# Kernel tuning notes

Hardware: AMD Instinct MI355X
Metric: run time of the kernel (lower is better)

Reference implementation:

```python
import jax, jax.numpy as jnp
import numpy as np

N_NODES = 50000


def gat_layer(x, src, dst, W, att_s, att_d, b, concat):
    # PyG GATConv (eval mode): h = x W reshaped to [N, H, C]
    H, C = att_s.shape
    h = (x @ W).reshape(-1, H, C)                      # [N, H, C]
    a_s = (h * att_s).sum(-1)                          # [N, H]
    a_d = (h * att_d).sum(-1)                          # [N, H]
    e = jax.nn.leaky_relu(a_s[src] + a_d[dst], 0.2)    # [E, H]
    # scatter-softmax over destination nodes
    m = jax.ops.segment_max(e, dst, num_segments=N_NODES)
    alpha = jnp.exp(e - m[dst])
    denom = jax.ops.segment_sum(alpha, dst, num_segments=N_NODES)
    alpha = alpha / denom[dst]                         # [E, H]
    msg = h[src] * alpha[:, :, None]                   # [E, H, C]
    out = jax.ops.segment_sum(msg, dst, num_segments=N_NODES)  # [N, H, C]
    out = out.reshape(N_NODES, H * C) if concat else out.mean(axis=1)
    return out + b


def setup_inputs() -> dict:
    key = jax.random.key(0)
    ks = jax.random.split(key, 16)
    F_IN, HID, HEADS, NCLS, E = 512, 64, 4, 40, 800000
    x = jax.random.normal(ks[0], (N_NODES, F_IN), dtype=jnp.float32)
    edge_index = jax.random.randint(ks[1], (2, E), 0, N_NODES, dtype=jnp.int32)

    def glorot(k, shape):
        fan = shape[0]
        return jax.random.normal(k, shape, dtype=jnp.float32) / np.sqrt(fan)

    d1 = HID * HEADS  # 256
    return {
        "x": x,
        "edge_index": edge_index,
        "W1": glorot(ks[2], (F_IN, d1)),
        "as1": glorot(ks[3], (HEADS, HID)),
        "ad1": glorot(ks[4], (HEADS, HID)),
        "b1": jnp.zeros((d1,), jnp.float32),
        "W2": glorot(ks[5], (d1, d1)),
        "as2": glorot(ks[6], (HEADS, HID)),
        "ad2": glorot(ks[7], (HEADS, HID)),
        "b2": jnp.zeros((d1,), jnp.float32),
        "W3": glorot(ks[8], (d1, NCLS)),
        "as3": glorot(ks[9], (1, NCLS)),
        "ad3": glorot(ks[10], (1, NCLS)),
        "b3": jnp.zeros((NCLS,), jnp.float32),
    }


def reference(x, edge_index, W1, as1, ad1, b1, W2, as2, ad2, b2, W3, as3, ad3, b3):
    # add self-loops (PyG GATConv default)
    loops = jnp.arange(N_NODES, dtype=edge_index.dtype)
    src = jnp.concatenate([edge_index[0], loops])
    dst = jnp.concatenate([edge_index[1], loops])
    h = jax.nn.elu(gat_layer(x, src, dst, W1, as1, ad1, b1, True))
    h = jax.nn.elu(gat_layer(h, src, dst, W2, as2, ad2, b2, True))
    out = gat_layer(h, src, dst, W3, as3, ad3, b3, False)
    return out
```

## Files before the change

### kernel.cpp

```cpp
#include <hip/hip_runtime.h>
#include <stdint.h>

#define NN 50000
#define NB 196

typedef unsigned short u16;
typedef _Float16 f16;
typedef __attribute__((ext_vector_type(8))) _Float16 half8;
typedef __attribute__((ext_vector_type(4))) _Float16 half4;
typedef __attribute__((ext_vector_type(4))) float f32x4;


__global__ void count_k(const int* __restrict__ dst, int* __restrict__ cnt, int E){
  int i = blockIdx.x * 256 + threadIdx.x;
  int tot = E + NN;
  if (i >= tot) return;
  int d = (i < E) ? dst[i] : (i - E);
  atomicAdd(&cnt[d], 1);
}

__global__ __launch_bounds__(256) void scan_part_k(const int* __restrict__ cnt,
                                                   int* __restrict__ bsum){
  __shared__ int lds[256];
  int tid = threadIdx.x;
  int idx = blockIdx.x * 256 + tid;
  lds[tid] = (idx < NN) ? cnt[idx] : 0;
  __syncthreads();
#pragma unroll
  for (int off = 128; off >= 1; off >>= 1){
    if (tid < off) lds[tid] += lds[tid + off];
    __syncthreads();
  }
  if (tid == 0) bsum[blockIdx.x] = lds[0];
}

__global__ __launch_bounds__(256) void scan_top_k(const int* __restrict__ bsum,
                                                  int* __restrict__ boff,
                                                  int* __restrict__ row_ptr){
  __shared__ int lds[256];
  int tid = threadIdx.x;
  int v = (tid < NB) ? bsum[tid] : 0;
  lds[tid] = v;
  __syncthreads();
#pragma unroll
  for (int off = 1; off < 256; off <<= 1){
    int t = (tid >= off) ? lds[tid - off] : 0;
    __syncthreads();
    lds[tid] += t;
    __syncthreads();
  }
  if (tid < NB) boff[tid] = lds[tid] - v;
  if (tid == 255) row_ptr[NN] = lds[255];
}

__global__ __launch_bounds__(256) void scan_fin_k(const int* __restrict__ cnt,
                                                  const int* __restrict__ boff,
                                                  int* __restrict__ row_ptr,
                                                  int* __restrict__ cursor){
  __shared__ int lds[256];
  int tid = threadIdx.x;
  int idx = blockIdx.x * 256 + tid;
  int v = (idx < NN) ? cnt[idx] : 0;
  lds[tid] = v;
  __syncthreads();
#pragma unroll
  for (int off = 1; off < 256; off <<= 1){
    int t = (tid >= off) ? lds[tid - off] : 0;
    __syncthreads();
    lds[tid] += t;
    __syncthreads();
  }
  if (idx < NN){
    int r = boff[blockIdx.x] + lds[tid] - v;
    row_ptr[idx] = r;
    cursor[idx]  = r;
  }
}

__global__ void scatter_k(const int* __restrict__ src, const int* __restrict__ dst,
                          int* __restrict__ cursor, int* __restrict__ csr, int E){
  int i = blockIdx.x * 256 + threadIdx.x;
  int tot = E + NN;
  if (i >= tot) return;
  int s, d;
  if (i < E){ s = src[i]; d = dst[i]; } else { s = i - E; d = i - E; }
  int pos = atomicAdd(&cursor[d], 1);
  csr[pos] = s;
}


__global__ void transpose_k(const float* __restrict__ W, f16* __restrict__ Wt, int K, int N){
  int i = blockIdx.x * 256 + threadIdx.x;
  if (i >= K * N) return;
  int n = i / K, k = i - n * K;
  Wt[i] = (f16)W[k * N + n];
}


template<bool A_FP32>
__global__ __launch_bounds__(256) void gemm_tile_k(const void* __restrict__ Aptr,
                                                   const f16* __restrict__ Bt,
                                                   f16* __restrict__ C,
                                                   int M, int N, int K){
  __shared__ f16 As[128 * 32];
  __shared__ f16 Bs[128 * 32];
  const int tid  = threadIdx.x;
  const int wave = tid >> 6, lane = tid & 63;
  const int quad = lane >> 4, l16 = lane & 15;
  const int wm = wave >> 1, wn = wave & 1;
  const int m0 = blockIdx.x * 128, n0 = blockIdx.y * 128;
  const int srow = tid >> 2;
  const int sc   = tid & 3;

  f32x4 acc[4][4] = {};

  for (int k0 = 0; k0 < K; k0 += 32){
#pragma unroll
    for (int rep = 0; rep < 2; rep++){
      int row = rep * 64 + srow;
      int gm = m0 + row;
      half8 va = {0,0,0,0,0,0,0,0};
      if (gm < M){
        if (A_FP32){
          const float* A = (const float*)Aptr + (size_t)gm * K + k0 + sc * 8;
          const f32x4 f0 = *(const f32x4*)(A);
          const f32x4 f1 = *(const f32x4*)(A + 4);
          va[0] = (f16)f0.x; va[1] = (f16)f0.y; va[2] = (f16)f0.z; va[3] = (f16)f0.w;
          va[4] = (f16)f1.x; va[5] = (f16)f1.y; va[6] = (f16)f1.z; va[7] = (f16)f1.w;
        } else {
          va = *(const half8*)((const f16*)Aptr + (size_t)gm * K + k0 + sc * 8);
        }
      }
      *(half8*)(&As[(((row >> 4) * 64) + sc * 16 + (row & 15)) * 8]) = va;
    }
#pragma unroll
    for (int rep = 0; rep < 2; rep++){
      int row = rep * 64 + srow;
      half8 vb = *(const half8*)(Bt + (size_t)(n0 + row) * K + k0 + sc * 8);
      *(half8*)(&Bs[(((row >> 4) * 64) + sc * 16 + (row & 15)) * 8]) = vb;
    }

    __syncthreads();
    half8 af[4], bf[4];
#pragma unroll
    for (int i = 0; i < 4; i++)
      af[i] = *(const half8*)(&As[((wm * 4 + i) * 64 + lane) * 8]);
#pragma unroll
    for (int j = 0; j < 4; j++)
      bf[j] = *(const half8*)(&Bs[((wn * 4 + j) * 64 + lane) * 8]);
#pragma unroll
    for (int i = 0; i < 4; i++)
#pragma unroll
      for (int j = 0; j < 4; j++)
        acc[i][j] = __builtin_amdgcn_mfma_f32_16x16x32_f16(af[i], bf[j], acc[i][j], 0, 0, 0);
    __syncthreads();
  }

#pragma unroll
  for (int i = 0; i < 4; i++){
#pragma unroll
    for (int j = 0; j < 4; j++){
      int n = n0 + (wn * 4 + j) * 16 + l16;
#pragma unroll
      for (int r = 0; r < 4; r++){
        int mm = m0 + (wm * 4 + i) * 16 + quad * 4 + r;
        if (mm < M) C[(size_t)mm * N + n] = (f16)acc[i][j][r];
      }
    }
  }
}


__global__ __launch_bounds__(256) void gemm_k(const f16* __restrict__ A,
                                              const f16* __restrict__ Bt,
                                              f16* __restrict__ C,
                                              int M, int N, int K){
  __shared__ f16 As[64 * 40];
  __shared__ f16 Bs[64 * 40];
  const int tid  = threadIdx.x;
  const int wave = tid >> 6, lane = tid & 63;
  const int quad = lane >> 4, l16 = lane & 15;
  const int m0 = blockIdx.x * 64, n0 = blockIdx.y * 64;
  const int srow = tid >> 2;
  const int scol = (tid & 3) * 8;

  f32x4 acc[4] = {};

  for (int k0 = 0; k0 < K; k0 += 32){
    half8 va = {0,0,0,0,0,0,0,0};
    int gm = m0 + srow;
    if (gm < M) va = *(const half8*)(A + (size_t)gm * K + k0 + scol);
    *(half8*)(&As[srow * 40 + scol]) = va;

    half8 vb = {0,0,0,0,0,0,0,0};
    int gn = n0 + srow;
    if (gn < N) vb = *(const half8*)(Bt + (size_t)gn * K + k0 + scol);
    *(half8*)(&Bs[srow * 40 + scol]) = vb;

    __syncthreads();
    half8 af = *(const half8*)(&As[(wave * 16 + l16) * 40 + quad * 8]);
#pragma unroll
    for (int i = 0; i < 4; i++){
      half8 bf = *(const half8*)(&Bs[(i * 16 + l16) * 40 + quad * 8]);
      acc[i] = __builtin_amdgcn_mfma_f32_16x16x32_f16(af, bf, acc[i], 0, 0, 0);
    }
    __syncthreads();
  }

#pragma unroll
  for (int i = 0; i < 4; i++){
    int n = n0 + i * 16 + l16;
#pragma unroll
    for (int r = 0; r < 4; r++){
      int m = m0 + wave * 16 + quad * 4 + r;
      if (m < M && n < N) C[(size_t)m * N + n] = (f16)acc[i][r];
    }
  }
}


__global__ __launch_bounds__(256) void attn4_k(const f16* __restrict__ h,
                                               const float* __restrict__ atts,
                                               const float* __restrict__ attd,
                                               float* __restrict__ a_s,
                                               float* __restrict__ a_d){
  int w = blockIdx.x * 4 + (threadIdx.x >> 6);
  if (w >= NN) return;
  int lane = threadIdx.x & 63;
  const half4 hv = *(const half4*)(h + (size_t)w * 256 + lane * 4);
  const f32x4 sv = *(const f32x4*)(atts + lane * 4);
  const f32x4 dv = *(const f32x4*)(attd + lane * 4);
  float h0 = (float)hv.x, h1 = (float)hv.y, h2 = (float)hv.z, h3 = (float)hv.w;
  float ps = h0 * sv.x + h1 * sv.y + h2 * sv.z + h3 * sv.w;
  float pd = h0 * dv.x + h1 * dv.y + h2 * dv.z + h3 * dv.w;
#pragma unroll
  for (int off = 8; off >= 1; off >>= 1){
    ps += __shfl_xor(ps, off);
    pd += __shfl_xor(pd, off);
  }
  if ((lane & 15) == 0){
    a_s[w * 4 + (lane >> 4)] = ps;
    a_d[w * 4 + (lane >> 4)] = pd;
  }
}

__global__ __launch_bounds__(256) void attn1_k(const f16* __restrict__ h,
                                               const float* __restrict__ atts,
                                               const float* __restrict__ attd,
                                               float* __restrict__ a_s,
                                               float* __restrict__ a_d){
  int w = blockIdx.x * 4 + (threadIdx.x >> 6);
  if (w >= NN) return;
  int lane = threadIdx.x & 63;
  float ps = 0.f, pd = 0.f;
  if (lane < 40){
    float hv = (float)h[(size_t)w * 40 + lane];
    ps = hv * atts[lane];
    pd = hv * attd[lane];
  }
#pragma unroll
  for (int off = 32; off >= 1; off >>= 1){
    ps += __shfl_xor(ps, off);
    pd += __shfl_xor(pd, off);
  }
  if (lane == 0){ a_s[w] = ps; a_d[w] = pd; }
}


__device__ __forceinline__ float lrelu(float e){ return e > 0.f ? e : 0.2f * e; }

__global__ __launch_bounds__(256) void agg4_k(const f16* __restrict__ h,
                                              const float* __restrict__ a_s,
                                              const float* __restrict__ a_d,
                                              const int* __restrict__ row_ptr,
                                              const int* __restrict__ csr,
                                              const float* __restrict__ bias,
                                              f16* __restrict__ out){
  int w = blockIdx.x * 4 + (threadIdx.x >> 6);
  if (w >= NN) return;
  int lane = threadIdx.x & 63;
  int head = lane >> 4;
  float ad = a_d[w * 4 + head];
  int beg = row_ptr[w], end = row_ptr[w + 1];

  float m = -1e30f, denom = 0.f;
  float acc0 = 0.f, acc1 = 0.f, acc2 = 0.f, acc3 = 0.f;

  int s0 = csr[beg];
  int s1 = csr[(beg + 1 < end) ? beg + 1 : beg];
  float e0 = a_s[s0 * 4 + head];
  float e1 = a_s[s1 * 4 + head];
  half4 h0 = *(const half4*)(h + (size_t)s0 * 256 + lane * 4);
  half4 h1 = *(const half4*)(h + (size_t)s1 * 256 + lane * 4);

  for (int j = beg; j < end; j += 2){
    int t0 = (j + 2 < end) ? j + 2 : j;
    int t1 = (j + 3 < end) ? j + 3 : j;
    int sp0 = csr[t0], sp1 = csr[t1];
    float ep0 = a_s[sp0 * 4 + head];
    float ep1 = a_s[sp1 * 4 + head];
    half4 hp0 = *(const half4*)(h + (size_t)sp0 * 256 + lane * 4);
    half4 hp1 = *(const half4*)(h + (size_t)sp1 * 256 + lane * 4);

    float ee0 = lrelu(e0 + ad);
    float ee1 = (j + 1 < end) ? lrelu(e1 + ad) : -1e30f;
    float mn = fmaxf(m, fmaxf(ee0, ee1));
    float cold = __expf(m - mn);
    float al0 = __expf(ee0 - mn);
    float al1 = __expf(ee1 - mn);
    denom = denom * cold + al0 + al1;
    acc0 = acc0 * cold + al0 * (float)h0.x + al1 * (float)h1.x;
    acc1 = acc1 * cold + al0 * (float)h0.y + al1 * (float)h1.y;
    acc2 = acc2 * cold + al0 * (float)h0.z + al1 * (float)h1.z;
    acc3 = acc3 * cold + al0 * (float)h0.w + al1 * (float)h1.w;
    m = mn;
    e0 = ep0; e1 = ep1; h0 = hp0; h1 = hp1;
  }

  float inv = 1.f / fmaxf(denom, 1e-30f);
  float o0 = acc0 * inv + bias[lane * 4 + 0];
  float o1 = acc1 * inv + bias[lane * 4 + 1];
  float o2 = acc2 * inv + bias[lane * 4 + 2];
  float o3 = acc3 * inv + bias[lane * 4 + 3];
  o0 = o0 > 0.f ? o0 : __expf(o0) - 1.f;
  o1 = o1 > 0.f ? o1 : __expf(o1) - 1.f;
  o2 = o2 > 0.f ? o2 : __expf(o2) - 1.f;
  o3 = o3 > 0.f ? o3 : __expf(o3) - 1.f;
  half4 r; r.x = (f16)o0; r.y = (f16)o1; r.z = (f16)o2; r.w = (f16)o3;
  *(half4*)(out + (size_t)w * 256 + lane * 4) = r;
}

__global__ __launch_bounds__(256) void agg1_k(const f16* __restrict__ h,
                                              const float* __restrict__ a_s,
                                              const float* __restrict__ a_d,
                                              const int* __restrict__ row_ptr,
                                              const int* __restrict__ csr,
                                              const float* __restrict__ bias,
                                              float* __restrict__ out){
  int w = blockIdx.x * 4 + (threadIdx.x >> 6);
  if (w >= NN) return;
  int lane = threadIdx.x & 63;
  int cl = (lane < 40) ? lane : 0;
  float ad = a_d[w];
  int beg = row_ptr[w], end = row_ptr[w + 1];

  float m = -1e30f, denom = 0.f, acc = 0.f;

  int s0 = csr[beg];
  int s1 = csr[(beg + 1 < end) ? beg + 1 : beg];
  float e0 = a_s[s0];
  float e1 = a_s[s1];
  float h0 = (float)h[(size_t)s0 * 40 + cl];
  float h1 = (float)h[(size_t)s1 * 40 + cl];

  for (int j = beg; j < end; j += 2){
    int t0 = (j + 2 < end) ? j + 2 : j;
    int t1 = (j + 3 < end) ? j + 3 : j;
    int sp0 = csr[t0], sp1 = csr[t1];
    float ep0 = a_s[sp0];
    float ep1 = a_s[sp1];
    float hp0 = (float)h[(size_t)sp0 * 40 + cl];
    float hp1 = (float)h[(size_t)sp1 * 40 + cl];

    float ee0 = lrelu(e0 + ad);
    float ee1 = (j + 1 < end) ? lrelu(e1 + ad) : -1e30f;
    float mn = fmaxf(m, fmaxf(ee0, ee1));
    float cold = __expf(m - mn);
    float al0 = __expf(ee0 - mn);
    float al1 = __expf(ee1 - mn);
    denom = denom * cold + al0 + al1;
    acc = acc * cold + al0 * h0 + al1 * h1;
    m = mn;
    e0 = ep0; e1 = ep1; h0 = hp0; h1 = hp1;
  }

  if (lane < 40){
    float o = acc / fmaxf(denom, 1e-30f) + bias[lane];
    out[(size_t)w * 40 + lane] = o;
  }
}


extern "C" void kernel_launch(void* const* d_in, const int* in_sizes, int n_in,
                              void* d_out, int out_size, void* d_ws, size_t ws_size,
                              hipStream_t stream){
  const float* x   = (const float*)d_in[0];
  const int*   ei  = (const int*)d_in[1];
  const float* W1  = (const float*)d_in[2];
  const float* as1 = (const float*)d_in[3];
  const float* ad1 = (const float*)d_in[4];
  const float* b1  = (const float*)d_in[5];
  const float* W2  = (const float*)d_in[6];
  const float* as2 = (const float*)d_in[7];
  const float* ad2 = (const float*)d_in[8];
  const float* b2  = (const float*)d_in[9];
  const float* W3  = (const float*)d_in[10];
  const float* as3 = (const float*)d_in[11];
  const float* ad3 = (const float*)d_in[12];
  const float* b3  = (const float*)d_in[13];

  const int E = in_sizes[1] / 2;
  const int ETOT = E + NN;
  const int* src_arr = ei;
  const int* dst_arr = ei + E;

  char* ws = (char*)d_ws;
  size_t off = 0;
  auto alloc = [&](size_t bytes) -> void* {
    void* p = ws + off; off += (bytes + 255) & ~(size_t)255; return p;
  };
  int*   cnt     = (int*)  alloc((size_t)NN * 4);
  int*   row_ptr = (int*)  alloc((size_t)(NN + 1) * 4);
  int*   cursor  = (int*)  alloc((size_t)NN * 4);
  int*   csr     = (int*)  alloc((size_t)ETOT * 4);
  int*   bsum    = (int*)  alloc((size_t)256 * 4);
  int*   boff    = (int*)  alloc((size_t)256 * 4);
  f16*   W1t     = (f16*)  alloc((size_t)512 * 256 * 2);
  f16*   W2t     = (f16*)  alloc((size_t)256 * 256 * 2);
  f16*   W3t     = (f16*)  alloc((size_t)256 * 40 * 2);
  float* a_s     = (float*)alloc((size_t)NN * 4 * 4);
  float* a_d     = (float*)alloc((size_t)NN * 4 * 4);
  f16*   hbuf    = (f16*)  alloc((size_t)NN * 256 * 2);
  f16*   xbuf    = (f16*)  alloc((size_t)NN * 256 * 2);
  (void)ws_size; (void)n_in; (void)out_size;

  hipMemsetAsync(cnt, 0, (size_t)NN * 4, stream);
  int egrid = (ETOT + 255) / 256;
  count_k    <<<egrid, 256, 0, stream>>>(dst_arr, cnt, E);
  scan_part_k<<<NB, 256, 0, stream>>>(cnt, bsum);
  scan_top_k <<<1, 256, 0, stream>>>(bsum, boff, row_ptr);
  scan_fin_k <<<NB, 256, 0, stream>>>(cnt, boff, row_ptr, cursor);
  scatter_k  <<<egrid, 256, 0, stream>>>(src_arr, dst_arr, cursor, csr, E);

  transpose_k<<<(512 * 256 + 255) / 256, 256, 0, stream>>>(W1, W1t, 512, 256);
  transpose_k<<<(256 * 256 + 255) / 256, 256, 0, stream>>>(W2, W2t, 256, 256);
  transpose_k<<<(256 * 40  + 255) / 256, 256, 0, stream>>>(W3, W3t, 256, 40);

  dim3 blk(256);
  dim3 gT((NN + 127) / 128, 2);
  dim3 gC((NN + 63) / 64, 1);
  int nodeblocks = (NN + 3) / 4;

  gemm_tile_k<true> <<<gT, blk, 0, stream>>>(x, W1t, hbuf, NN, 256, 512);
  attn4_k<<<nodeblocks, blk, 0, stream>>>(hbuf, as1, ad1, a_s, a_d);
  agg4_k <<<nodeblocks, blk, 0, stream>>>(hbuf, a_s, a_d, row_ptr, csr, b1, xbuf);

  gemm_tile_k<false><<<gT, blk, 0, stream>>>(xbuf, W2t, hbuf, NN, 256, 256);
  attn4_k<<<nodeblocks, blk, 0, stream>>>(hbuf, as2, ad2, a_s, a_d);
  agg4_k <<<nodeblocks, blk, 0, stream>>>(hbuf, a_s, a_d, row_ptr, csr, b2, xbuf);

  gemm_k<<<gC, blk, 0, stream>>>(xbuf, W3t, hbuf, NN, 40, 256);
  attn1_k<<<nodeblocks, blk, 0, stream>>>(hbuf, as3, ad3, a_s, a_d);
  agg1_k <<<nodeblocks, blk, 0, stream>>>(hbuf, a_s, a_d, row_ptr, csr, b3, (float*)d_out);
}
```

Measured before the change: 561.3 us.

## Fuse attention-logit dot products into GEMM epilogues and double-buffer GEMM via direct LDS loads

Computes a_s and a_d inside the GEMM epilogues from the fp32 accumulators, so the separate attn4_k and attn1_k passes that reread h are removed. The big-tile GEMM is also restructured to use global_load_lds direct-to-LDS copies with double buffering, overlapping the next K-slice load with MFMA work. For the fp32 input layer, fp32 values now go into LDS and are converted when fragments are read, which doubles the A-tile LDS footprint. Logits are now taken from unrounded fp32 accumulators rather than from the fp16-stored h.

```diff
diff --git a/kernel.cpp b/kernel.cpp
--- a/kernel.cpp
+++ b/kernel.cpp
@@ -9,6 +9,13 @@
 typedef __attribute__((ext_vector_type(8))) _Float16 half8;
 typedef __attribute__((ext_vector_type(4))) _Float16 half4;
 typedef __attribute__((ext_vector_type(4))) float f32x4;
+
+__device__ __forceinline__ void gload_lds16(const void* gsrc, void* ldst){
+  __builtin_amdgcn_global_load_lds(
+      (const __attribute__((address_space(1))) unsigned int*)gsrc,
+      (__attribute__((address_space(3))) unsigned int*)ldst,
+      16, 0, 0);
+}
 
 
 __global__ void count_k(const int* __restrict__ dst, int* __restrict__ cnt, int E){
@@ -98,73 +105,143 @@
 
 
 template<bool A_FP32>
-__global__ __launch_bounds__(256) void gemm_tile_k(const void* __restrict__ Aptr,
-                                                   const f16* __restrict__ Bt,
-                                                   f16* __restrict__ C,
-                                                   int M, int N, int K){
-  __shared__ f16 As[128 * 32];
-  __shared__ f16 Bs[128 * 32];
+__global__ __launch_bounds__(256) void gemm_tile2_k(const void* __restrict__ Aptr,
+                                                    const f16* __restrict__ Bt,
+                                                    f16* __restrict__ C,
+                                                    const float* __restrict__ atts,
+                                                    const float* __restrict__ attd,
+                                                    float* __restrict__ a_s,
+                                                    float* __restrict__ a_d,
+                                                    int M, int N, int K){
+  constexpr int ABYTES = A_FP32 ? 16384 : 8192;
+  constexpr int STEPB  = ABYTES + 8192;
+  __shared__ __attribute__((aligned(16))) char lds[2 * STEPB];
+
   const int tid  = threadIdx.x;
   const int wave = tid >> 6, lane = tid & 63;
   const int quad = lane >> 4, l16 = lane & 15;
   const int wm = wave >> 1, wn = wave & 1;
   const int m0 = blockIdx.x * 128, n0 = blockIdx.y * 128;
-  const int srow = tid >> 2;
-  const int sc   = tid & 3;
+  const int sc_l = lane >> 4, r_l = lane & 15;
+
+  size_t bsrc[2]; int bdst[2];
+#pragma unroll
+  for (int j = 0; j < 2; ++j){
+    int nt = wave * 2 + j;
+    bsrc[j] = (size_t)(n0 + nt * 16 + r_l) * K + sc_l * 8;
+    bdst[j] = (wave * 128 + j * 64) * 16;
+  }
+  size_t asrc[4]; int adst[4];
+  if constexpr (A_FP32){
+#pragma unroll
+    for (int j = 0; j < 4; ++j){
+      int mt = wave * 2 + (j & 1);
+      int h  = j >> 1;
+      int row = m0 + mt * 16 + r_l; if (row > M - 1) row = M - 1;
+      asrc[j] = (size_t)row * K + sc_l * 8 + h * 4;
+      adst[j] = h * 8192 + mt * 1024;
+    }
+  } else {
+#pragma unroll
+    for (int j = 0; j < 2; ++j){
+      int mt = wave * 2 + j;
+      int row = m0 + mt * 16 + r_l; if (row > M - 1) row = M - 1;
+      asrc[j] = (size_t)row * K + sc_l * 8;
+      adst[j] = mt * 1024;
+      asrc[j + 2] = 0; adst[j + 2] = 0;
+    }
+  }
+
+  auto stage = [&](int buf, int k0){
+    char* Ab  = lds + buf * STEPB;
+    char* Bb  = Ab + ABYTES;
+    if constexpr (A_FP32){
+      const float* A = (const float*)Aptr;
+#pragma unroll
+      for (int j = 0; j < 4; ++j)
+        gload_lds16(A + asrc[j] + k0, Ab + adst[j]);
+    } else {
+      const f16* A = (const f16*)Aptr;
+#pragma unroll
+      for (int j = 0; j < 2; ++j)
+        gload_lds16(A + asrc[j] + k0, Ab + adst[j]);
+    }
+#pragma unroll
+    for (int j = 0; j < 2; ++j)
+      gload_lds16(Bt + bsrc[j] + k0, Bb + bdst[j]);
+  };
 
   f32x4 acc[4][4] = {};
 
-  for (int k0 = 0; k0 < K; k0 += 32){
-#pragma unroll
-    for (int rep = 0; rep < 2; rep++){
-      int row = rep * 64 + srow;
-      int gm = m0 + row;
-      half8 va = {0,0,0,0,0,0,0,0};
-      if (gm < M){
-        if (A_FP32){
-          const float* A = (const float*)Aptr + (size_t)gm * K + k0 + sc * 8;
-          const f32x4 f0 = *(const f32x4*)(A);
-          const f32x4 f1 = *(const f32x4*)(A + 4);
-          va[0] = (f16)f0.x; va[1] = (f16)f0.y; va[2] = (f16)f0.z; va[3] = (f16)f0.w;
-          va[4] = (f16)f1.x; va[5] = (f16)f1.y; va[6] = (f16)f1.z; va[7] = (f16)f1.w;
-        } else {
-          va = *(const half8*)((const f16*)Aptr + (size_t)gm * K + k0 + sc * 8);
-        }
+  stage(0, 0);
+  asm volatile("s_waitcnt vmcnt(0)" ::: "memory");
+  __syncthreads();
+
+  const int nk = K >> 5;
+  int cur = 0;
+  for (int t = 0; t < nk; ++t){
+    if (t + 1 < nk) stage(cur ^ 1, (t + 1) << 5);
+
+    char* Ab = lds + cur * STEPB;
+    f16*  Bb = (f16*)(Ab + ABYTES);
+    half8 af[4], bf[4];
+    if constexpr (A_FP32){
+#pragma unroll
+      for (int i = 0; i < 4; ++i){
+        const f32x4 lo = *(const f32x4*)(Ab + (((wm * 4 + i) * 64 + lane) * 16));
+        const f32x4 hi = *(const f32x4*)(Ab + 8192 + (((wm * 4 + i) * 64 + lane) * 16));
+        half8 v;
+        v[0] = (f16)lo.x; v[1] = (f16)lo.y; v[2] = (f16)lo.z; v[3] = (f16)lo.w;
+        v[4] = (f16)hi.x; v[5] = (f16)hi.y; v[6] = (f16)hi.z; v[7] = (f16)hi.w;
+        af[i] = v;
       }
-      *(half8*)(&As[(((row >> 4) * 64) + sc * 16 + (row & 15)) * 8]) = va;
-    }
-#pragma unroll
-    for (int rep = 0; rep < 2; rep++){
-      int row = rep * 64 + srow;
-      half8 vb = *(const half8*)(Bt + (size_t)(n0 + row) * K + k0 + sc * 8);
-      *(half8*)(&Bs[(((row >> 4) * 64) + sc * 16 + (row & 15)) * 8]) = vb;
-    }
-
-    __syncthreads();
-    half8 af[4], bf[4];
-#pragma unroll
-    for (int i = 0; i < 4; i++)
-      af[i] = *(const half8*)(&As[((wm * 4 + i) * 64 + lane) * 8]);
-#pragma unroll
-    for (int j = 0; j < 4; j++)
-      bf[j] = *(const half8*)(&Bs[((wn * 4 + j) * 64 + lane) * 8]);
-#pragma unroll
-    for (int i = 0; i < 4; i++)
-#pragma unroll
-      for (int j = 0; j < 4; j++)
+    } else {
+#pragma unroll
+      for (int i = 0; i < 4; ++i)
+        af[i] = *(const half8*)(Ab + (((wm * 4 + i) * 64 + lane) * 16));
+    }
+#pragma unroll
+    for (int j = 0; j < 4; ++j)
+      bf[j] = *(const half8*)((char*)Bb + (((wn * 4 + j) * 64 + lane) * 16));
+#pragma unroll
+    for (int i = 0; i < 4; ++i)
+#pragma unroll
+      for (int j = 0; j < 4; ++j)
         acc[i][j] = __builtin_amdgcn_mfma_f32_16x16x32_f16(af[i], bf[j], acc[i][j], 0, 0, 0);
-    __syncthreads();
-  }
-
-#pragma unroll
-  for (int i = 0; i < 4; i++){
-#pragma unroll
-    for (int j = 0; j < 4; j++){
-      int n = n0 + (wn * 4 + j) * 16 + l16;
-#pragma unroll
-      for (int r = 0; r < 4; r++){
-        int mm = m0 + (wm * 4 + i) * 16 + quad * 4 + r;
-        if (mm < M) C[(size_t)mm * N + n] = (f16)acc[i][j][r];
+
+    __syncthreads();
+    cur ^= 1;
+  }
+
+  const int head = blockIdx.y * 2 + wn;
+  float sA[4], dA[4];
+#pragma unroll
+  for (int j = 0; j < 4; ++j){
+    sA[j] = atts[head * 64 + j * 16 + l16];
+    dA[j] = attd[head * 64 + j * 16 + l16];
+  }
+#pragma unroll
+  for (int i = 0; i < 4; ++i){
+#pragma unroll
+    for (int r = 0; r < 4; ++r){
+      int mm = m0 + (wm * 4 + i) * 16 + quad * 4 + r;
+      float vs = 0.f, vd = 0.f;
+#pragma unroll
+      for (int j = 0; j < 4; ++j){
+        float v = acc[i][j][r];
+        vs += v * sA[j];
+        vd += v * dA[j];
+        int n = n0 + (wn * 4 + j) * 16 + l16;
+        if (mm < M) C[(size_t)mm * N + n] = (f16)v;
+      }
+#pragma unroll
+      for (int off = 8; off >= 1; off >>= 1){
+        vs += __shfl_xor(vs, off);
+        vd += __shfl_xor(vd, off);
+      }
+      if (l16 == 0 && mm < M){
+        a_s[mm * 4 + head] = vs;
+        a_d[mm * 4 + head] = vd;
       }
     }
   }
@@ -174,6 +251,10 @@
 __global__ __launch_bounds__(256) void gemm_k(const f16* __restrict__ A,
                                               const f16* __restrict__ Bt,
                                               f16* __restrict__ C,
+                                              const float* __restrict__ atts,
+                                              const float* __restrict__ attd,
+                                              float* __restrict__ a_s,
+                                              float* __restrict__ a_d,
                                               int M, int N, int K){
   __shared__ f16 As[64 * 40];
   __shared__ f16 Bs[64 * 40];
@@ -216,54 +297,33 @@
       if (m < M && n < N) C[(size_t)m * N + n] = (f16)acc[i][r];
     }
   }
-}
-
-
-__global__ __launch_bounds__(256) void attn4_k(const f16* __restrict__ h,
-                                               const float* __restrict__ atts,
-                                               const float* __restrict__ attd,
-                                               float* __restrict__ a_s,
-                                               float* __restrict__ a_d){
-  int w = blockIdx.x * 4 + (threadIdx.x >> 6);
-  if (w >= NN) return;
-  int lane = threadIdx.x & 63;
-  const half4 hv = *(const half4*)(h + (size_t)w * 256 + lane * 4);
-  const f32x4 sv = *(const f32x4*)(atts + lane * 4);
-  const f32x4 dv = *(const f32x4*)(attd + lane * 4);
-  float h0 = (float)hv.x, h1 = (float)hv.y, h2 = (float)hv.z, h3 = (float)hv.w;
-  float ps = h0 * sv.x + h1 * sv.y + h2 * sv.z + h3 * sv.w;
-  float pd = h0 * dv.x + h1 * dv.y + h2 * dv.z + h3 * dv.w;
-#pragma unroll
-  for (int off = 8; off >= 1; off >>= 1){
-    ps += __shfl_xor(ps, off);
-    pd += __shfl_xor(pd, off);
-  }
-  if ((lane & 15) == 0){
-    a_s[w * 4 + (lane >> 4)] = ps;
-    a_d[w * 4 + (lane >> 4)] = pd;
-  }
-}
-
-__global__ __launch_bounds__(256) void attn1_k(const f16* __restrict__ h,
-                                               const float* __restrict__ atts,
-                                               const float* __restrict__ attd,
-                                               float* __restrict__ a_s,
-                                               float* __restrict__ a_d){
-  int w = blockIdx.x * 4 + (threadIdx.x >> 6);
-  if (w >= NN) return;
-  int lane = threadIdx.x & 63;
-  float ps = 0.f, pd = 0.f;
-  if (lane < 40){
-    float hv = (float)h[(size_t)w * 40 + lane];
-    ps = hv * atts[lane];
-    pd = hv * attd[lane];
-  }
-#pragma unroll
-  for (int off = 32; off >= 1; off >>= 1){
-    ps += __shfl_xor(ps, off);
-    pd += __shfl_xor(pd, off);
-  }
-  if (lane == 0){ a_s[w] = ps; a_d[w] = pd; }
+
+  float sA[4], dA[4];
+#pragma unroll
+  for (int i = 0; i < 4; i++){
+    int n = n0 + i * 16 + l16;
+    sA[i] = (n < N) ? atts[n] : 0.f;
+    dA[i] = (n < N) ? attd[n] : 0.f;
+  }
+#pragma unroll
+  for (int r = 0; r < 4; r++){
+    float vs = 0.f, vd = 0.f;
+#pragma unroll
+    for (int i = 0; i < 4; i++){
+      vs += acc[i][r] * sA[i];
+      vd += acc[i][r] * dA[i];
+    }
+#pragma unroll
+    for (int off = 8; off >= 1; off >>= 1){
+      vs += __shfl_xor(vs, off);
+      vd += __shfl_xor(vd, off);
+    }
+    int m = m0 + wave * 16 + quad * 4 + r;
+    if (l16 == 0 && m < M){
+      a_s[m] = vs;
+      a_d[m] = vd;
+    }
+  }
 }
 
 
@@ -441,15 +501,12 @@
   dim3 gC((NN + 63) / 64, 1);
   int nodeblocks = (NN + 3) / 4;
 
-  gemm_tile_k<true> <<<gT, blk, 0, stream>>>(x, W1t, hbuf, NN, 256, 512);
-  attn4_k<<<nodeblocks, blk, 0, stream>>>(hbuf, as1, ad1, a_s, a_d);
+  gemm_tile2_k<true> <<<gT, blk, 0, stream>>>(x, W1t, hbuf, as1, ad1, a_s, a_d, NN, 256, 512);
   agg4_k <<<nodeblocks, blk, 0, stream>>>(hbuf, a_s, a_d, row_ptr, csr, b1, xbuf);
 
-  gemm_tile_k<false><<<gT, blk, 0, stream>>>(xbuf, W2t, hbuf, NN, 256, 256);
-  attn4_k<<<nodeblocks, blk, 0, stream>>>(hbuf, as2, ad2, a_s, a_d);
+  gemm_tile2_k<false><<<gT, blk, 0, stream>>>(xbuf, W2t, hbuf, as2, ad2, a_s, a_d, NN, 256, 256);
   agg4_k <<<nodeblocks, blk, 0, stream>>>(hbuf, a_s, a_d, row_ptr, csr, b2, xbuf);
 
-  gemm_k<<<gC, blk, 0, stream>>>(xbuf, W3t, hbuf, NN, 40, 256);
-  attn1_k<<<nodeblocks, blk, 0, stream>>>(hbuf, as3, ad3, a_s, a_d);
+  gemm_k<<<gC, blk, 0, stream>>>(xbuf, W3t, hbuf, as3, ad3, a_s, a_d, NN, 40, 256);
   agg1_k <<<nodeblocks, blk, 0, stream>>>(hbuf, a_s, a_d, row_ptr, csr, b3, (float*)d_out);
 }
```

New measurement: 549.7 us. 2.1% less time.
